# Optimization experiments

Measured on AMD Instinct MI355X. Metric: run time of the kernel, lower is better.

Reference implementation:

```python
import jax, jax.numpy as jnp
import numpy as np

B, T, D, H, d = 2, 2048, 1024, 16, 64
INNER = H * d
SCALE = d ** -0.5


def _rope(x, inv_freq):
    # x: [B, H, T, d], interleaved rotary as in the torch module
    t = x.shape[2]
    pos = jnp.arange(t, dtype=jnp.float32)
    freqs = pos[:, None] * inv_freq[None, :]          # [T, d/2]
    cos_f, sin_f = jnp.cos(freqs), jnp.sin(freqs)
    x1, x2 = x[..., 0::2], x[..., 1::2]
    y1 = x1 * cos_f - x2 * sin_f
    y2 = x1 * sin_f + x2 * cos_f
    return jnp.stack([y1, y2], axis=-1).reshape(x.shape)


def setup_inputs() -> dict:
    key = jax.random.key(0)
    ks = jax.random.split(key, 6)
    x = jax.random.normal(ks[0], (B, T, D), jnp.float32)
    W_qkv = jax.random.normal(ks[1], (D, 3 * INNER), jnp.float32) * (D ** -0.5)
    W_out = jax.random.normal(ks[2], (INNER, D), jnp.float32) * (INNER ** -0.5)
    W_dt = jax.random.normal(ks[3], (D, H), jnp.float32) * 0.01
    b_dt = jnp.full((H,), -4.0, jnp.float32)
    W_gsp = jax.random.normal(ks[4], (D, INNER), jnp.float32) * 0.01
    b_gsp = jnp.full((INNER,), -3.0, jnp.float32)
    inv_freq = 1.0 / (10000.0 ** (jnp.arange(0, d, 2, dtype=jnp.float32) / d))
    return {"x": x, "W_qkv": W_qkv, "W_out": W_out, "W_dt": W_dt,
            "b_dt": b_dt, "W_gsp": W_gsp, "b_gsp": b_gsp, "inv_freq": inv_freq}


def reference(x, W_qkv, W_out, W_dt, b_dt, W_gsp, b_gsp, inv_freq):
    qkv = (x @ W_qkv).reshape(B, T, 3, H, d)
    Q = jnp.moveaxis(qkv[:, :, 0], 1, 2)   # [B,H,T,d]
    K = jnp.moveaxis(qkv[:, :, 1], 1, 2)
    V = jnp.moveaxis(qkv[:, :, 2], 1, 2)
    Q = _rope(Q, inv_freq)
    K = _rope(K, inv_freq)

    dt = jax.nn.softplus(x @ W_dt + b_dt)             # [B,T,H]
    gamma = jnp.moveaxis(jnp.exp(-dt), 1, 2)          # [B,H,T]

    p = jax.nn.sigmoid(x @ W_gsp + b_gsp).reshape(B, T, H, d)
    p = jnp.moveaxis(p, 1, 2)                          # [B,H,T,d]
    gamma_eff = gamma[..., None] * (1.0 - p) + p
    gamma_scalar = gamma_eff.mean(axis=-1)            # [B,H,T]
    V = V * (1.0 - p)

    log_gamma = jnp.log(jnp.clip(gamma_scalar, 1e-6, 1.0 - 1e-6))
    lgc = jnp.cumsum(log_gamma, axis=-1)              # [B,H,T]
    log_D = jnp.clip(lgc[..., :, None] - lgc[..., None, :], -20.0, 0.0)
    causal = jnp.tril(jnp.ones((T, T), jnp.float32))
    Dm = jnp.exp(log_D) * causal                      # [B,H,T,T]

    Wscore = jnp.einsum('bhtd,bhsd->bhts', Q * SCALE, K)
    A = Wscore * Dm
    Y = jnp.einsum('bhts,bhsd->bhtd', A, V)
    Y = jnp.moveaxis(Y, 1, 2).reshape(B, T, INNER)
    return Y @ W_out
```

## Files before the change

### kernel.cpp

```cpp
#include <hip/hip_runtime.h>
#include <hip/hip_bf16.h>
#include <math.h>

#define B_     2
#define T_     2048
#define D_     1024
#define H_     16
#define INNER_ 1024
#define NC_    4096
#define SCALE_ 0.125f

typedef unsigned short u16;
typedef short short8 __attribute__((ext_vector_type(8)));
typedef float f32x4 __attribute__((ext_vector_type(4)));
typedef unsigned short u16x4 __attribute__((ext_vector_type(4)));

__device__ __forceinline__ u16 f2bf(float x) {
  union { float f; unsigned u; } v; v.f = x;
  unsigned r = v.u + 0x7fffu + ((v.u >> 16) & 1u);
  return (u16)(r >> 16);
}
__device__ __forceinline__ float b2f(u16 x) {
  union { unsigned u; float f; } v; v.u = ((unsigned)x) << 16;
  return v.f;
}
__device__ __forceinline__ void gload16(const void* g, void* l) {
  __builtin_amdgcn_global_load_lds(
      (const __attribute__((address_space(1))) void*)g,
      (__attribute__((address_space(3))) void*)l, 16, 0, 0);
}

__global__ __launch_bounds__(256) void prep_kernel(
    const float* __restrict__ x, const float* __restrict__ W_qkv,
    const float* __restrict__ W_gsp, const float* __restrict__ W_out,
    const float* __restrict__ W_dt, const float* __restrict__ inv_freq,
    u16* __restrict__ xb, u16* __restrict__ Wcombt, u16* __restrict__ Woutt,
    u16* __restrict__ Wdtb, float2* __restrict__ tab) {
  const int bid = blockIdx.x, tid = threadIdx.x;
  if (bid < 1280) {
    const float* src; u16* dst; int N, nx, ky;
    if (bid < 768)       { src = W_qkv; dst = Wcombt;                N = 3072; nx = bid % 48;          ky = bid / 48; }
    else if (bid < 1024) { src = W_gsp; dst = Wcombt + 3072 * 1024;  N = 1024; nx = (bid - 768) % 16;  ky = (bid - 768) / 16; }
    else                 { src = W_out; dst = Woutt;                 N = 1024; nx = (bid - 1024) % 16; ky = (bid - 1024) / 16; }
    __shared__ float tile[64][65];
    const int k0 = ky * 64, n0 = nx * 64;
    for (int e = tid; e < 4096; e += 256) {
      int kk = e >> 6, nn = e & 63;
      tile[kk][nn] = src[(size_t)(k0 + kk) * N + n0 + nn];
    }
    __syncthreads();
    for (int e = tid; e < 4096; e += 256) {
      int nn = e >> 6, kk = e & 63;
      dst[(size_t)(n0 + nn) * 1024 + k0 + kk] = f2bf(tile[kk][nn]);
    }
  } else if (bid < 1344) {
    int i = (bid - 1280) * 256 + tid;
    int k = i >> 4, h = i & 15;
    Wdtb[(size_t)h * D_ + k] = f2bf(W_dt[i]);
  } else if (bid < 1600) {
    int i = (bid - 1344) * 256 + tid;
    int t = i >> 5, j = i & 31;
    float s, c;
    sincosf((float)t * inv_freq[j], &s, &c);
    tab[i] = make_float2(c, s);
  } else {
    int base = (bid - 1600) * 1024 + tid;
#pragma unroll
    for (int r = 0; r < 4; ++r) {
      int i = base + r * 256;
      float4 v = *reinterpret_cast<const float4*>(x + (size_t)i * 4);
      u16x4 o; o.x = f2bf(v.x); o.y = f2bf(v.y); o.z = f2bf(v.z); o.w = f2bf(v.w);
      *reinterpret_cast<u16x4*>(xb + (size_t)i * 4) = o;
    }
  }
}

__global__ __launch_bounds__(256) void gamma_kernel(
    const u16* __restrict__ xb, const u16* __restrict__ Wdtb,
    const float* __restrict__ b_dt, float* __restrict__ gam) {
  const int row = blockIdx.x * 4 + (threadIdx.x >> 6);
  const int l = threadIdx.x & 63;
  const int h = l >> 2;
  const int kc = (l & 3) * 256;
  const short8* xp = (const short8*)(xb + (size_t)row * D_ + kc);
  const short8* wp = (const short8*)(Wdtb + h * D_ + kc);
  float s = 0.f;
#pragma unroll
  for (int i = 0; i < 32; ++i) {
    short8 xv = xp[i], wv = wp[i];
#pragma unroll
    for (int j = 0; j < 8; ++j) s += b2f((u16)xv[j]) * b2f((u16)wv[j]);
  }
  s += __shfl_xor(s, 1);
  s += __shfl_xor(s, 2);
  if ((l & 3) == 0) {
    float v = s + b_dt[h];
    float sp = (v > 20.f) ? v : log1pf(__expf(v));
    gam[row * H_ + h] = __expf(-sp);
  }
}

#define SWZG(r) ((((r) & 3) ^ (((r) >> 2) & 1)))

__device__ __forceinline__ void stage_op(const u16* __restrict__ gbase, int kt,
                                         char* ldst, int h, int tid) {
  int r = h * 128 + (tid >> 2);
  int kg = (tid & 3) ^ SWZG(r);
  gload16(gbase + (size_t)r * D_ + kt * 32 + kg * 8,
          ldst + (h * 128 + (tid >> 6) * 16) * 64);
}
__device__ __forceinline__ short8 ldfrag(const char* tile, int row, int g4) {
  return *(const short8*)(tile + row * 64 + ((g4 ^ SWZG(row)) << 4));
}

__global__ __launch_bounds__(512, 2) void gemm_big(
    const u16* __restrict__ A, const u16* __restrict__ Bt,
    u16* __restrict__ C) {
  __shared__ char lds[4 * 32768];
  const int tid = threadIdx.x;
  const int w = tid >> 6, l = tid & 63;
  const int bid = blockIdx.x;
  const int xcd = bid & 7, idx = bid >> 3;
  const int brow = (xcd >> 1) * 4 + (idx & 3);
  const int bcol = (xcd & 1) * 8 + (idx >> 2);
  const int m0 = brow * 256, n0 = bcol * 256;
  const int wr = (w >> 2) * 128, wc = (w & 3) * 64;
  const int ql = l & 15, g4 = l >> 4;

  const u16* Ag = A + (size_t)m0 * D_;
  const u16* Bg = Bt + (size_t)n0 * D_;

  f32x4 acc[8][4] = {};

#pragma unroll
  for (int t = 0; t < 3; ++t) {
    char* bufA = lds + t * 32768;
    char* bufB = bufA + 16384;
    stage_op(Ag, t, bufA, 0, tid); stage_op(Ag, t, bufA, 1, tid);
    stage_op(Bg, t, bufB, 0, tid); stage_op(Bg, t, bufB, 1, tid);
  }

  const int NT = D_ / 32;
  for (int kt = 0; kt < NT; ++kt) {
    if (kt < NT - 2)       asm volatile("s_waitcnt vmcnt(8)" ::: "memory");
    else if (kt == NT - 2) asm volatile("s_waitcnt vmcnt(4)" ::: "memory");
    else                   asm volatile("s_waitcnt vmcnt(0)" ::: "memory");
    __builtin_amdgcn_sched_barrier(0);
    __builtin_amdgcn_s_barrier();
    __builtin_amdgcn_sched_barrier(0);

    char* bufA = lds + (kt & 3) * 32768;
    char* bufB = bufA + 16384;
    char* nbufA = lds + ((kt + 3) & 3) * 32768;
    char* nbufB = nbufA + 16384;
    const bool pre = (kt + 3 < NT);

    if (pre) {
      stage_op(Ag, kt + 3, nbufA, 0, tid);
      stage_op(Ag, kt + 3, nbufA, 1, tid);
    }
    short8 bf[4];
#pragma unroll
    for (int nf = 0; nf < 4; ++nf) bf[nf] = ldfrag(bufB, wc + nf * 16 + ql, g4);
    short8 af[4];
#pragma unroll
    for (int mf = 0; mf < 4; ++mf) af[mf] = ldfrag(bufA, wr + mf * 16 + ql, g4);
    __builtin_amdgcn_s_setprio(1);
#pragma unroll
    for (int mf = 0; mf < 4; ++mf)
#pragma unroll
      for (int nf = 0; nf < 4; ++nf)
        acc[mf][nf] = __builtin_amdgcn_mfma_f32_16x16x32_bf16(af[mf], bf[nf], acc[mf][nf], 0, 0, 0);
    __builtin_amdgcn_s_setprio(0);

    if (pre) {
      stage_op(Bg, kt + 3, nbufB, 0, tid);
      stage_op(Bg, kt + 3, nbufB, 1, tid);
    }
    short8 af2[4];
#pragma unroll
    for (int mf = 0; mf < 4; ++mf) af2[mf] = ldfrag(bufA, wr + 64 + mf * 16 + ql, g4);
    __builtin_amdgcn_s_setprio(1);
#pragma unroll
    for (int mf = 0; mf < 4; ++mf)
#pragma unroll
      for (int nf = 0; nf < 4; ++nf)
        acc[mf + 4][nf] = __builtin_amdgcn_mfma_f32_16x16x32_bf16(af2[mf], bf[nf], acc[mf + 4][nf], 0, 0, 0);
    __builtin_amdgcn_s_setprio(0);
  }

#pragma unroll
  for (int mf = 0; mf < 8; ++mf) {
#pragma unroll
    for (int r = 0; r < 4; ++r) {
      size_t row = (size_t)(m0 + wr + mf * 16 + g4 * 4 + r);
      size_t base = row * NC_ + n0 + wc + ql;
#pragma unroll
      for (int nf = 0; nf < 4; ++nf)
        C[base + nf * 16] = f2bf(acc[mf][nf][r]);
    }
  }
}

template <bool BF16OUT>
__global__ __launch_bounds__(256) void gemm_bt(
    const u16* __restrict__ A, const u16* __restrict__ Bt,
    void* __restrict__ Cv, int M, int N, int K) {
  __shared__ u16 As[2][128 * 64] __attribute__((aligned(16)));
  __shared__ u16 Bs[2][128 * 64] __attribute__((aligned(16)));
  const int tid = threadIdx.x, w = tid >> 6, l = tid & 63;
  const int rpx = (M >> 7) >> 3;
  const int bid = blockIdx.x;
  const int xcd = bid & 7, idx = bid >> 3;
  const int brow = xcd * rpx + (idx % rpx);
  const int bcol = idx / rpx;
  const int m0 = brow * 128, n0 = bcol * 128;
  const int wr = (w >> 1) * 64, wc = (w & 1) * 64;
  const int srow = l >> 3;
  const int kgrp = ((l & 7) ^ srow) * 8;

  f32x4 acc[4][4] = {};

  auto stage = [&](int kt, int bs) {
#pragma unroll
    for (int i = 0; i < 4; ++i) {
      int c = w * 4 + i;
      int row = c * 8 + srow;
      gload16(A + (size_t)(m0 + row) * K + kt * 64 + kgrp, (char*)As[bs] + c * 1024);
      gload16(Bt + (size_t)(n0 + row) * K + kt * 64 + kgrp, (char*)Bs[bs] + c * 1024);
    }
  };

  stage(0, 0);
  const int NT = K >> 6;
  for (int kt = 0; kt < NT; ++kt) {
    if (kt + 1 < NT) {
      stage(kt + 1, (kt + 1) & 1);
      asm volatile("s_waitcnt vmcnt(8)" ::: "memory");
    } else {
      asm volatile("s_waitcnt vmcnt(0)" ::: "memory");
    }
    __builtin_amdgcn_sched_barrier(0);
    __builtin_amdgcn_s_barrier();
    __builtin_amdgcn_sched_barrier(0);
    const char* Asb = (const char*)As[kt & 1];
    const char* Bsb = (const char*)Bs[kt & 1];
#pragma unroll
    for (int kk = 0; kk < 2; ++kk) {
      short8 af[4], bf[4];
#pragma unroll
      for (int i = 0; i < 4; ++i) {
        int ra = wr + i * 16 + (l & 15);
        int sa = kk * 4 + (l >> 4);
        af[i] = *(const short8*)(Asb + ra * 128 + ((sa ^ (ra & 7)) << 4));
        int rb = wc + i * 16 + (l & 15);
        bf[i] = *(const short8*)(Bsb + rb * 128 + ((sa ^ (rb & 7)) << 4));
      }
#pragma unroll
      for (int i = 0; i < 4; ++i)
#pragma unroll
        for (int j = 0; j < 4; ++j)
          acc[i][j] = __builtin_amdgcn_mfma_f32_16x16x32_bf16(af[i], bf[j], acc[i][j], 0, 0, 0);
    }
    if (kt + 1 < NT) __builtin_amdgcn_s_barrier();
  }
#pragma unroll
  for (int i = 0; i < 4; ++i) {
#pragma unroll
    for (int r = 0; r < 4; ++r) {
      size_t row = (size_t)(m0 + wr + i * 16 + (l >> 4) * 4 + r);
      size_t base = row * N + n0 + wc + (l & 15);
#pragma unroll
      for (int j = 0; j < 4; ++j) {
        if (BF16OUT) ((u16*)Cv)[base + j * 16] = f2bf(acc[i][j][r]);
        else         ((float*)Cv)[base + j * 16] = acc[i][j][r];
      }
    }
  }
}

__global__ __launch_bounds__(256) void pointwise_kernel(
    const u16* __restrict__ C, const float* __restrict__ gam,
    const float* __restrict__ b_gsp, const float2* __restrict__ tab,
    u16* __restrict__ Qb, u16* __restrict__ Kb, u16* __restrict__ Vb,
    float* __restrict__ lg) {
  const int row = blockIdx.x * 4 + (threadIdx.x >> 6);
  const int l = threadIdx.x & 63;
  const int b = row >> 11, t = row & (T_ - 1);
  const int h = l >> 2;
  const int dd0 = (l & 3) * 16;
  const int col = h * 64 + dd0;
  const size_t cb = (size_t)row * NC_;

  const float gh = gam[row * H_ + h];
  const short8* qp = (const short8*)(C + cb + col);
  const short8* kp = (const short8*)(C + cb + 1024 + col);
  const short8* vp = (const short8*)(C + cb + 2048 + col);
  const short8* pp = (const short8*)(C + cb + 3072 + col);
  short8 q0 = qp[0], q1 = qp[1];
  short8 k0 = kp[0], k1 = kp[1];
  short8 v0 = vp[0], v1 = vp[1];
  short8 pr0 = pp[0], pr1 = pp[1];

  float ge = 0.f;
  short8 vo0, vo1;
#pragma unroll
  for (int i = 0; i < 8; ++i) {
    float pv = b2f((u16)pr0[i]) + b_gsp[col + i];
    float p = 1.f / (1.f + __expf(-pv));
    ge += gh * (1.f - p) + p;
    vo0[i] = (short)f2bf(b2f((u16)v0[i]) * (1.f - p));
    float pv1 = b2f((u16)pr1[i]) + b_gsp[col + 8 + i];
    float p1 = 1.f / (1.f + __expf(-pv1));
    ge += gh * (1.f - p1) + p1;
    vo1[i] = (short)f2bf(b2f((u16)v1[i]) * (1.f - p1));
  }
  const size_t hm = (((size_t)(b * H_ + h)) * T_ + t) * 64 + dd0;
  ((short8*)(Vb + hm))[0] = vo0;
  ((short8*)(Vb + hm))[1] = vo1;

  ge += __shfl_xor(ge, 1);
  ge += __shfl_xor(ge, 2);
  if ((l & 3) == 0) {
    float gs = ge * (1.f / 64.f);
    gs = fminf(fmaxf(gs, 1e-6f), 1.f - 1e-6f);
    lg[((size_t)(b * H_ + h)) * T_ + t] = logf(gs);
  }

  short8 qo0, qo1, ko0, ko1;
  const float2* cs = tab + t * 32 + (dd0 >> 1);
#pragma unroll
  for (int m = 0; m < 4; ++m) {
    float2 c0 = cs[m];
    float qa = b2f((u16)q0[2 * m]), qb = b2f((u16)q0[2 * m + 1]);
    qo0[2 * m]     = (short)f2bf((qa * c0.x - qb * c0.y) * SCALE_);
    qo0[2 * m + 1] = (short)f2bf((qa * c0.y + qb * c0.x) * SCALE_);
    float ka = b2f((u16)k0[2 * m]), kb = b2f((u16)k0[2 * m + 1]);
    ko0[2 * m]     = (short)f2bf(ka * c0.x - kb * c0.y);
    ko0[2 * m + 1] = (short)f2bf(ka * c0.y + kb * c0.x);
    float2 c1 = cs[4 + m];
    float qa1 = b2f((u16)q1[2 * m]), qb1 = b2f((u16)q1[2 * m + 1]);
    qo1[2 * m]     = (short)f2bf((qa1 * c1.x - qb1 * c1.y) * SCALE_);
    qo1[2 * m + 1] = (short)f2bf((qa1 * c1.y + qb1 * c1.x) * SCALE_);
    float ka1 = b2f((u16)k1[2 * m]), kb1 = b2f((u16)k1[2 * m + 1]);
    ko1[2 * m]     = (short)f2bf(ka1 * c1.x - kb1 * c1.y);
    ko1[2 * m + 1] = (short)f2bf(ka1 * c1.y + kb1 * c1.x);
  }
  ((short8*)(Qb + hm))[0] = qo0; ((short8*)(Qb + hm))[1] = qo1;
  ((short8*)(Kb + hm))[0] = ko0; ((short8*)(Kb + hm))[1] = ko1;
}

__global__ __launch_bounds__(256) void scan_kernel(
    const float* __restrict__ lg, float* __restrict__ lgc) {
  const size_t base = (size_t)blockIdx.x * T_;
  const int tid = threadIdx.x;
  __shared__ float sums[256];
  float loc[8];
  float run = 0.f;
#pragma unroll
  for (int i = 0; i < 8; ++i) { run += lg[base + tid * 8 + i]; loc[i] = run; }
  sums[tid] = run;
  __syncthreads();
  if (tid == 0) {
    float r = 0.f;
    for (int i = 0; i < 256; ++i) { float v = sums[i]; sums[i] = r; r += v; }
  }
  __syncthreads();
  const float off = sums[tid];
#pragma unroll
  for (int i = 0; i < 8; ++i) lgc[base + tid * 8 + i] = off + loc[i];
}

__global__ __launch_bounds__(256) void kv_prep_kernel(
    const u16* __restrict__ Vb, const float* __restrict__ lgc,
    u16* __restrict__ Vtg) {
  const int stile = blockIdx.x;
  const int bh = blockIdx.y;
  const int tid = threadIdx.x;
  __shared__ u16 vt[64][72];
  const size_t base = ((size_t)bh * T_ + (size_t)stile * 64) * 64;
  const float* lgp = lgc + (size_t)bh * T_;
  const float lgb = lgp[stile * 64];
#pragma unroll
  for (int i = 0; i < 2; ++i) {
    int c = tid * 2 + i;
    int row = c >> 3, k8 = (c & 7) * 8;
    float beta = __expf(lgb - lgp[stile * 64 + row]);
    short8 vv = *(const short8*)(Vb + base + row * 64 + k8);
#pragma unroll
    for (int j = 0; j < 8; ++j) vt[row][k8 + j] = f2bf(b2f((u16)vv[j]) * beta);
  }
  __syncthreads();
#pragma unroll
  for (int i = 0; i < 2; ++i) {
    int c = tid * 2 + i;
    int dd = c >> 3, t8 = (c & 7) * 8;
    short8 o;
#pragma unroll
    for (int j = 0; j < 8; ++j) o[j] = (short)vt[t8 + j][dd];
    *(short8*)(Vtg + ((size_t)bh * 64 + dd) * T_ + stile * 64 + t8) = o;
  }
}

__global__ __launch_bounds__(256) void attn_mfma(
    const u16* __restrict__ Qb, const u16* __restrict__ Kb,
    const u16* __restrict__ Vtg, const float* __restrict__ lgc,
    u16* __restrict__ Y) {
  const int i = blockIdx.x;
  const int tt = (i >> 3) & 31;
  const int bh = (i & 7) + ((i >> 8) << 3);
  const int b = bh >> 4, h = bh & 15;
  const int tid = threadIdx.x, w = tid >> 6, l = tid & 63;
  __shared__ u16 Qs[64 * 64] __attribute__((aligned(16)));
  __shared__ u16 Ks[2][64 * 64] __attribute__((aligned(16)));
  __shared__ u16 Vs[2][64 * 64] __attribute__((aligned(16)));
  const u16* Qg = Qb + (size_t)bh * T_ * 64;
  const u16* Kg = Kb + (size_t)bh * T_ * 64;
  const u16* Vg = Vtg + (size_t)bh * 64 * T_;
  const float* lgp = lgc + (size_t)bh * T_;

  const int srow = l >> 3;
  const int kgrp = ((l & 7) ^ srow) * 8;
  const int ql = l & 15, g4 = l >> 4;

#pragma unroll
  for (int i2 = 0; i2 < 2; ++i2) {
    int c = w * 2 + i2;
    int row = c * 8 + srow;
    gload16(Qg + (size_t)(tt * 64 + row) * 64 + kgrp, (char*)Qs + c * 1024);
  }
  const float lgq = lgp[tt * 64 + w * 16 + ql];
  const float lgtop = lgp[tt * 64];
  __syncthreads();

  short8 qf[2];
#pragma unroll
  for (int kk = 0; kk < 2; ++kk) {
    int row = w * 16 + ql;
    int slot = kk * 4 + g4;
    qf[kk] = *(const short8*)((const char*)Qs + row * 128 + ((slot ^ (row & 7)) << 4));
  }
  char* Pw = (char*)Qs + w * 2048;
  const int pswz = (ql & 7) << 4;

  f32x4 yacc[4] = {};

  {
    const int bs = tt & 1;
#pragma unroll
    for (int i2 = 0; i2 < 2; ++i2) {
      int c = w * 2 + i2, row = c * 8 + srow;
      gload16(Kg + (size_t)(tt * 64 + row) * 64 + kgrp, (char*)Ks[bs] + c * 1024);
      gload16(Vg + (size_t)row * T_ + tt * 64 + kgrp, (char*)Vs[bs] + c * 1024);
    }
  }

  for (int st = tt;; --st) {
    const int bs = st & 1;
    const bool last = (st == 0) || (lgtop - lgp[(st - 1) * 64 + 63] <= -20.f);
    if (!last) {
#pragma unroll
      for (int i2 = 0; i2 < 2; ++i2) {
        int c = w * 2 + i2, row = c * 8 + srow;
        gload16(Kg + (size_t)((st - 1) * 64 + row) * 64 + kgrp, (char*)Ks[bs ^ 1] + c * 1024);
        gload16(Vg + (size_t)row * T_ + (st - 1) * 64 + kgrp, (char*)Vs[bs ^ 1] + c * 1024);
      }
      asm volatile("s_waitcnt vmcnt(4)" ::: "memory");
    } else {
      asm volatile("s_waitcnt vmcnt(0)" ::: "memory");
    }
    __builtin_amdgcn_sched_barrier(0);
    __builtin_amdgcn_s_barrier();
    __builtin_amdgcn_sched_barrier(0);

    const float alpha = __expf(lgq - lgp[st * 64]);
    const bool diag = (st == tt);
    const char* Ksb = (const char*)Ks[bs];
    const char* Vsb = (const char*)Vs[bs];
#pragma unroll
    for (int n = 0; n < 4; ++n) {
      f32x4 s = {};
#pragma unroll
      for (int kk = 0; kk < 2; ++kk) {
        int row = n * 16 + ql;
        int slot = kk * 4 + g4;
        short8 kf = *(const short8*)(Ksb + row * 128 + ((slot ^ (row & 7)) << 4));
        s = __builtin_amdgcn_mfma_f32_16x16x32_bf16(kf, qf[kk], s, 0, 0, 0);
      }
      u16x4 pk;
#pragma unroll
      for (int r = 0; r < 4; ++r) {
        float pv = s[r] * alpha;
        if (diag && (n * 16 + g4 * 4 + r) > (w * 16 + ql)) pv = 0.f;
        pk[r] = f2bf(pv);
      }
      *(u16x4*)(Pw + ((ql * 128 + n * 32 + g4 * 8) ^ pswz)) = pk;
    }
#pragma unroll
    for (int kk = 0; kk < 2; ++kk) {
      short8 pf = *(const short8*)(Pw + ((ql * 128 + kk * 64 + g4 * 16) ^ pswz));
#pragma unroll
      for (int n2 = 0; n2 < 4; ++n2) {
        int row = n2 * 16 + ql;
        int slot = kk * 4 + g4;
        short8 vf = *(const short8*)(Vsb + row * 128 + ((slot ^ (row & 7)) << 4));
        yacc[n2] = __builtin_amdgcn_mfma_f32_16x16x32_bf16(pf, vf, yacc[n2], 0, 0, 0);
      }
    }
    if (last) break;
    __builtin_amdgcn_s_barrier();
  }

#pragma unroll
  for (int n2 = 0; n2 < 4; ++n2)
#pragma unroll
    for (int r = 0; r < 4; ++r) {
      size_t row = (size_t)(b * T_) + tt * 64 + w * 16 + g4 * 4 + r;
      Y[row * INNER_ + h * 64 + n2 * 16 + ql] = f2bf(yacc[n2][r]);
    }
}

extern "C" void kernel_launch(void* const* d_in, const int* in_sizes, int n_in,
                              void* d_out, int out_size, void* d_ws, size_t ws_size,
                              hipStream_t stream) {
  const float* x        = (const float*)d_in[0];
  const float* W_qkv    = (const float*)d_in[1];
  const float* W_out    = (const float*)d_in[2];
  const float* W_dt     = (const float*)d_in[3];
  const float* b_dt     = (const float*)d_in[4];
  const float* W_gsp    = (const float*)d_in[5];
  const float* b_gsp    = (const float*)d_in[6];
  const float* inv_freq = (const float*)d_in[7];
  float* out = (float*)d_out;

  const int M = B_ * T_;
  char* p = (char*)d_ws;
  auto alloc = [&](size_t bytes) {
    char* r = p; p += (bytes + 255) & ~(size_t)255; return r;
  };
  u16*    xb    = (u16*)alloc((size_t)M * D_ * 2);
  u16*    Wcombt= (u16*)alloc((size_t)NC_ * D_ * 2);
  u16*    Woutt = (u16*)alloc((size_t)D_ * INNER_ * 2);
  u16*    Wdtb  = (u16*)alloc((size_t)H_ * D_ * 2);
  u16*    Cqkvp = (u16*)alloc((size_t)M * NC_ * 2);
  u16*    Qb    = (u16*)alloc((size_t)B_ * H_ * T_ * 64 * 2);
  u16*    Kb    = (u16*)alloc((size_t)B_ * H_ * T_ * 64 * 2);
  u16*    Vb    = (u16*)alloc((size_t)B_ * H_ * T_ * 64 * 2);
  float*  gam   = (float*)alloc((size_t)M * H_ * 4);
  float*  lg    = (float*)alloc((size_t)B_ * H_ * T_ * 4);
  float*  lgc   = (float*)alloc((size_t)B_ * H_ * T_ * 4);
  float2* tab   = (float2*)alloc((size_t)T_ * 32 * 8);
  u16*    Vtg   = Cqkvp;
  u16*    Yb    = Cqkvp + (size_t)4 * 1024 * 1024;

  prep_kernel<<<2624, 256, 0, stream>>>(x, W_qkv, W_gsp, W_out, W_dt, inv_freq,
                                        xb, Wcombt, Woutt, Wdtb, tab);
  gamma_kernel<<<M / 4, 256, 0, stream>>>(xb, Wdtb, b_dt, gam);
  gemm_big<<<256, 512, 0, stream>>>(xb, Wcombt, Cqkvp);

  pointwise_kernel<<<M / 4, 256, 0, stream>>>(Cqkvp, gam, b_gsp, tab,
                                              Qb, Kb, Vb, lg);
  scan_kernel<<<B_ * H_, 256, 0, stream>>>(lg, lgc);
  kv_prep_kernel<<<dim3(T_ / 64, B_ * H_), 256, 0, stream>>>(Vb, lgc, Vtg);

  attn_mfma<<<1024, 256, 0, stream>>>(Qb, Kb, Vtg, lgc, Yb);

  gemm_bt<false><<<256, 256, 0, stream>>>(Yb, Woutt, out, M, D_, INNER_);
}
```

Baseline: 156.2 us.

## Load K/V fragments directly from global into registers, drop LDS staging

The attention kernel no longer stages Q, K and V tiles through shared memory with double buffering and block barriers. Each wave now loads its MFMA operand fragments straight from global memory into registers, and the V-transpose kernel writes V in a tiled [bh][tile][d][64] layout so those loads are contiguous. It also raises wave priority around MFMA sections. This removes the LDS traffic and barriers, but gives up explicit prefetch overlap and has every wave re-read the full K/V tiles from global memory or cache.

```diff
diff --git a/kernel.cpp b/kernel.cpp
--- a/kernel.cpp
+++ b/kernel.cpp
@@ -398,7 +398,7 @@
     short8 o;
 #pragma unroll
     for (int j = 0; j < 8; ++j) o[j] = (short)vt[t8 + j][dd];
-    *(short8*)(Vtg + ((size_t)bh * 64 + dd) * T_ + stile * 64 + t8) = o;
+    *(short8*)(Vtg + ((size_t)(bh * 32 + stile) * 64 + dd) * 64 + t8) = o;
   }
 }
 
@@ -411,82 +411,47 @@
   const int bh = (i & 7) + ((i >> 8) << 3);
   const int b = bh >> 4, h = bh & 15;
   const int tid = threadIdx.x, w = tid >> 6, l = tid & 63;
-  __shared__ u16 Qs[64 * 64] __attribute__((aligned(16)));
-  __shared__ u16 Ks[2][64 * 64] __attribute__((aligned(16)));
-  __shared__ u16 Vs[2][64 * 64] __attribute__((aligned(16)));
+  __shared__ u16 Ps[4][1024];
   const u16* Qg = Qb + (size_t)bh * T_ * 64;
   const u16* Kg = Kb + (size_t)bh * T_ * 64;
-  const u16* Vg = Vtg + (size_t)bh * 64 * T_;
+  const u16* Vg = Vtg + (size_t)bh * 32 * 4096;
   const float* lgp = lgc + (size_t)bh * T_;
-
-  const int srow = l >> 3;
-  const int kgrp = ((l & 7) ^ srow) * 8;
   const int ql = l & 15, g4 = l >> 4;
 
-#pragma unroll
-  for (int i2 = 0; i2 < 2; ++i2) {
-    int c = w * 2 + i2;
-    int row = c * 8 + srow;
-    gload16(Qg + (size_t)(tt * 64 + row) * 64 + kgrp, (char*)Qs + c * 1024);
-  }
+  const u16* qptr = Qg + (size_t)(tt * 64 + w * 16 + ql) * 64 + g4 * 8;
+  const short8 qf0 = *(const short8*)(qptr);
+  const short8 qf1 = *(const short8*)(qptr + 32);
   const float lgq = lgp[tt * 64 + w * 16 + ql];
   const float lgtop = lgp[tt * 64];
-  __syncthreads();
-
-  short8 qf[2];
-#pragma unroll
-  for (int kk = 0; kk < 2; ++kk) {
-    int row = w * 16 + ql;
-    int slot = kk * 4 + g4;
-    qf[kk] = *(const short8*)((const char*)Qs + row * 128 + ((slot ^ (row & 7)) << 4));
-  }
-  char* Pw = (char*)Qs + w * 2048;
+
+  char* Pw = (char*)Ps[w];
   const int pswz = (ql & 7) << 4;
 
   f32x4 yacc[4] = {};
 
-  {
-    const int bs = tt & 1;
-#pragma unroll
-    for (int i2 = 0; i2 < 2; ++i2) {
-      int c = w * 2 + i2, row = c * 8 + srow;
-      gload16(Kg + (size_t)(tt * 64 + row) * 64 + kgrp, (char*)Ks[bs] + c * 1024);
-      gload16(Vg + (size_t)row * T_ + tt * 64 + kgrp, (char*)Vs[bs] + c * 1024);
-    }
-  }
-
-  for (int st = tt;; --st) {
-    const int bs = st & 1;
-    const bool last = (st == 0) || (lgtop - lgp[(st - 1) * 64 + 63] <= -20.f);
-    if (!last) {
-#pragma unroll
-      for (int i2 = 0; i2 < 2; ++i2) {
-        int c = w * 2 + i2, row = c * 8 + srow;
-        gload16(Kg + (size_t)((st - 1) * 64 + row) * 64 + kgrp, (char*)Ks[bs ^ 1] + c * 1024);
-        gload16(Vg + (size_t)row * T_ + (st - 1) * 64 + kgrp, (char*)Vs[bs ^ 1] + c * 1024);
-      }
-      asm volatile("s_waitcnt vmcnt(4)" ::: "memory");
-    } else {
-      asm volatile("s_waitcnt vmcnt(0)" ::: "memory");
-    }
-    __builtin_amdgcn_sched_barrier(0);
-    __builtin_amdgcn_s_barrier();
-    __builtin_amdgcn_sched_barrier(0);
-
+  for (int st = tt; st >= 0; --st) {
+    if (st < tt && lgtop - lgp[st * 64 + 63] <= -20.f) break;
+    const u16* kb = Kg + (size_t)st * 64 * 64;
+    const u16* vb = Vg + (size_t)st * 4096;
+    short8 kf[4][2], vf[4][2];
+#pragma unroll
+    for (int n = 0; n < 4; ++n) {
+      const u16* kr = kb + (n * 16 + ql) * 64 + g4 * 8;
+      kf[n][0] = *(const short8*)(kr);
+      kf[n][1] = *(const short8*)(kr + 32);
+      const u16* vr = vb + (n * 16 + ql) * 64 + g4 * 8;
+      vf[n][0] = *(const short8*)(vr);
+      vf[n][1] = *(const short8*)(vr + 32);
+    }
     const float alpha = __expf(lgq - lgp[st * 64]);
     const bool diag = (st == tt);
-    const char* Ksb = (const char*)Ks[bs];
-    const char* Vsb = (const char*)Vs[bs];
 #pragma unroll
     for (int n = 0; n < 4; ++n) {
       f32x4 s = {};
-#pragma unroll
-      for (int kk = 0; kk < 2; ++kk) {
-        int row = n * 16 + ql;
-        int slot = kk * 4 + g4;
-        short8 kf = *(const short8*)(Ksb + row * 128 + ((slot ^ (row & 7)) << 4));
-        s = __builtin_amdgcn_mfma_f32_16x16x32_bf16(kf, qf[kk], s, 0, 0, 0);
-      }
+      __builtin_amdgcn_s_setprio(1);
+      s = __builtin_amdgcn_mfma_f32_16x16x32_bf16(kf[n][0], qf0, s, 0, 0, 0);
+      s = __builtin_amdgcn_mfma_f32_16x16x32_bf16(kf[n][1], qf1, s, 0, 0, 0);
+      __builtin_amdgcn_s_setprio(0);
       u16x4 pk;
 #pragma unroll
       for (int r = 0; r < 4; ++r) {
@@ -499,16 +464,12 @@
 #pragma unroll
     for (int kk = 0; kk < 2; ++kk) {
       short8 pf = *(const short8*)(Pw + ((ql * 128 + kk * 64 + g4 * 16) ^ pswz));
-#pragma unroll
-      for (int n2 = 0; n2 < 4; ++n2) {
-        int row = n2 * 16 + ql;
-        int slot = kk * 4 + g4;
-        short8 vf = *(const short8*)(Vsb + row * 128 + ((slot ^ (row & 7)) << 4));
-        yacc[n2] = __builtin_amdgcn_mfma_f32_16x16x32_bf16(pf, vf, yacc[n2], 0, 0, 0);
-      }
-    }
-    if (last) break;
-    __builtin_amdgcn_s_barrier();
+      __builtin_amdgcn_s_setprio(1);
+#pragma unroll
+      for (int n2 = 0; n2 < 4; ++n2)
+        yacc[n2] = __builtin_amdgcn_mfma_f32_16x16x32_bf16(pf, vf[n2][kk], yacc[n2], 0, 0, 0);
+      __builtin_amdgcn_s_setprio(0);
+    }
   }
 
 #pragma unroll
```

After: 255.3 us. +63.5%, slower.

## Use 32x32 MFMA with 128-row query tiles and tiled V layout in attention

Applied to the files above, without the earlier changes.

The attention kernel now handles 128 query rows per block (32 per wave) using 32x32x16 bf16 MFMA instead of 16x16x32, which halves the grid and lets each loaded K/V tile serve twice as many queries. Q fragments are loaded straight from global memory instead of being staged through LDS. The transposed V buffer is rewritten as contiguous 64x64 tiles so each tile is read from one contiguous 8 KB region. Fully masked diagonal tiles are skipped and s_setprio hints wrap the MFMA sections. The trade-off is more registers per wave and fewer blocks in flight for the causal workload.

```diff
diff --git a/kernel.cpp b/kernel.cpp
--- a/kernel.cpp
+++ b/kernel.cpp
@@ -13,6 +13,7 @@
 typedef unsigned short u16;
 typedef short short8 __attribute__((ext_vector_type(8)));
 typedef float f32x4 __attribute__((ext_vector_type(4)));
+typedef float f32x16 __attribute__((ext_vector_type(16)));
 typedef unsigned short u16x4 __attribute__((ext_vector_type(4)));
 
 __device__ __forceinline__ u16 f2bf(float x) {
@@ -398,7 +399,7 @@
     short8 o;
 #pragma unroll
     for (int j = 0; j < 8; ++j) o[j] = (short)vt[t8 + j][dd];
-    *(short8*)(Vtg + ((size_t)bh * 64 + dd) * T_ + stile * 64 + t8) = o;
+    *(short8*)(Vtg + ((size_t)(bh * 32 + stile) * 64 + dd) * 64 + t8) = o;
   }
 }
 
@@ -407,63 +408,57 @@
     const u16* __restrict__ Vtg, const float* __restrict__ lgc,
     u16* __restrict__ Y) {
   const int i = blockIdx.x;
-  const int tt = (i >> 3) & 31;
-  const int bh = (i & 7) + ((i >> 8) << 3);
+  const int xcd = i & 7, r = i >> 3;
+  const int qb = r & 15;
+  const int bh = xcd + ((r >> 4) << 3);
   const int b = bh >> 4, h = bh & 15;
   const int tid = threadIdx.x, w = tid >> 6, l = tid & 63;
-  __shared__ u16 Qs[64 * 64] __attribute__((aligned(16)));
+  const int l31 = l & 31, hi = l >> 5;
   __shared__ u16 Ks[2][64 * 64] __attribute__((aligned(16)));
   __shared__ u16 Vs[2][64 * 64] __attribute__((aligned(16)));
+  __shared__ u16 Ps[4][2048] __attribute__((aligned(16)));
   const u16* Qg = Qb + (size_t)bh * T_ * 64;
   const u16* Kg = Kb + (size_t)bh * T_ * 64;
-  const u16* Vg = Vtg + (size_t)bh * 64 * T_;
+  const u16* Vg = Vtg + (size_t)bh * 32 * 4096;
   const float* lgp = lgc + (size_t)bh * T_;
-
-  const int srow = l >> 3;
-  const int kgrp = ((l & 7) ^ srow) * 8;
-  const int ql = l & 15, g4 = l >> 4;
-
-#pragma unroll
-  for (int i2 = 0; i2 < 2; ++i2) {
-    int c = w * 2 + i2;
-    int row = c * 8 + srow;
-    gload16(Qg + (size_t)(tt * 64 + row) * 64 + kgrp, (char*)Qs + c * 1024);
-  }
-  const float lgq = lgp[tt * 64 + w * 16 + ql];
-  const float lgtop = lgp[tt * 64];
-  __syncthreads();
-
-  short8 qf[2];
-#pragma unroll
-  for (int kk = 0; kk < 2; ++kk) {
-    int row = w * 16 + ql;
-    int slot = kk * 4 + g4;
-    qf[kk] = *(const short8*)((const char*)Qs + row * 128 + ((slot ^ (row & 7)) << 4));
-  }
-  char* Pw = (char*)Qs + w * 2048;
-  const int pswz = (ql & 7) << 4;
-
-  f32x4 yacc[4] = {};
-
+  const int srow = l >> 3, slot8 = l & 7;
+
+  const int q0 = qb * 128 + w * 32;
+  const int qg = q0 + l31;
+  short8 qf[4];
+#pragma unroll
+  for (int kk = 0; kk < 4; ++kk)
+    qf[kk] = *(const short8*)(Qg + (size_t)qg * 64 + kk * 16 + hi * 8);
+  const float lgq = lgp[qg];
+  const float lgtop = lgp[qb * 128];
+
+  char* Pw = (char*)Ps[w];
+  const int psw = l31 & 7;
+
+  f32x16 yacc0 = {}, yacc1 = {};
+
+  const int st0 = qb * 2 + 1;
   {
-    const int bs = tt & 1;
+    const int bs = st0 & 1;
 #pragma unroll
     for (int i2 = 0; i2 < 2; ++i2) {
       int c = w * 2 + i2, row = c * 8 + srow;
-      gload16(Kg + (size_t)(tt * 64 + row) * 64 + kgrp, (char*)Ks[bs] + c * 1024);
-      gload16(Vg + (size_t)row * T_ + tt * 64 + kgrp, (char*)Vs[bs] + c * 1024);
-    }
-  }
-
-  for (int st = tt;; --st) {
+      int kg = (slot8 ^ (row & 7)) * 8;
+      gload16(Kg + (size_t)(st0 * 64 + row) * 64 + kg, (char*)Ks[bs] + c * 1024);
+      gload16(Vg + (size_t)st0 * 4096 + row * 64 + kg, (char*)Vs[bs] + c * 1024);
+    }
+  }
+
+  for (int st = st0;; --st) {
     const int bs = st & 1;
     const bool last = (st == 0) || (lgtop - lgp[(st - 1) * 64 + 63] <= -20.f);
     if (!last) {
 #pragma unroll
       for (int i2 = 0; i2 < 2; ++i2) {
         int c = w * 2 + i2, row = c * 8 + srow;
-        gload16(Kg + (size_t)((st - 1) * 64 + row) * 64 + kgrp, (char*)Ks[bs ^ 1] + c * 1024);
-        gload16(Vg + (size_t)row * T_ + (st - 1) * 64 + kgrp, (char*)Vs[bs ^ 1] + c * 1024);
+        int kg = (slot8 ^ (row & 7)) * 8;
+        gload16(Kg + (size_t)((st - 1) * 64 + row) * 64 + kg, (char*)Ks[bs ^ 1] + c * 1024);
+        gload16(Vg + (size_t)(st - 1) * 4096 + row * 64 + kg, (char*)Vs[bs ^ 1] + c * 1024);
       }
       asm volatile("s_waitcnt vmcnt(4)" ::: "memory");
     } else {
@@ -473,38 +468,47 @@
     __builtin_amdgcn_s_barrier();
     __builtin_amdgcn_sched_barrier(0);
 
-    const float alpha = __expf(lgq - lgp[st * 64]);
-    const bool diag = (st == tt);
-    const char* Ksb = (const char*)Ks[bs];
-    const char* Vsb = (const char*)Vs[bs];
-#pragma unroll
-    for (int n = 0; n < 4; ++n) {
-      f32x4 s = {};
-#pragma unroll
-      for (int kk = 0; kk < 2; ++kk) {
-        int row = n * 16 + ql;
-        int slot = kk * 4 + g4;
-        short8 kf = *(const short8*)(Ksb + row * 128 + ((slot ^ (row & 7)) << 4));
-        s = __builtin_amdgcn_mfma_f32_16x16x32_bf16(kf, qf[kk], s, 0, 0, 0);
+    const bool allinv = (st * 64 > q0 + 31);
+    if (!allinv) {
+      const char* Ksb = (const char*)Ks[bs];
+      const char* Vsb = (const char*)Vs[bs];
+      const float alpha = __expf(lgq - lgp[st * 64]);
+      const bool domask = (st * 64 + 63 > q0);
+      const int qrel = qg - st * 64;
+#pragma unroll
+      for (int sblk = 0; sblk < 2; ++sblk) {
+        f32x16 c = {};
+        __builtin_amdgcn_s_setprio(1);
+#pragma unroll
+        for (int kk = 0; kk < 4; ++kk) {
+          int row = sblk * 32 + l31;
+          short8 kf = *(const short8*)(Ksb + row * 128 + (((kk * 2 + hi) ^ (row & 7)) << 4));
+          c = __builtin_amdgcn_mfma_f32_32x32x16_bf16(kf, qf[kk], c, 0, 0, 0);
+        }
+        __builtin_amdgcn_s_setprio(0);
+#pragma unroll
+        for (int bq = 0; bq < 4; ++bq) {
+          u16x4 pk;
+#pragma unroll
+          for (int r2 = 0; r2 < 4; ++r2) {
+            int s64 = sblk * 32 + bq * 8 + hi * 4 + r2;
+            float pv = c[bq * 4 + r2] * alpha;
+            if (domask && s64 > qrel) pv = 0.f;
+            pk[r2] = f2bf(pv);
+          }
+          int slot = sblk * 4 + bq;
+          *(u16x4*)(Pw + l31 * 128 + ((slot ^ psw) << 4) + hi * 8) = pk;
+        }
       }
-      u16x4 pk;
-#pragma unroll
-      for (int r = 0; r < 4; ++r) {
-        float pv = s[r] * alpha;
-        if (diag && (n * 16 + g4 * 4 + r) > (w * 16 + ql)) pv = 0.f;
-        pk[r] = f2bf(pv);
-      }
-      *(u16x4*)(Pw + ((ql * 128 + n * 32 + g4 * 8) ^ pswz)) = pk;
-    }
-#pragma unroll
-    for (int kk = 0; kk < 2; ++kk) {
-      short8 pf = *(const short8*)(Pw + ((ql * 128 + kk * 64 + g4 * 16) ^ pswz));
-#pragma unroll
-      for (int n2 = 0; n2 < 4; ++n2) {
-        int row = n2 * 16 + ql;
-        int slot = kk * 4 + g4;
-        short8 vf = *(const short8*)(Vsb + row * 128 + ((slot ^ (row & 7)) << 4));
-        yacc[n2] = __builtin_amdgcn_mfma_f32_16x16x32_bf16(pf, vf, yacc[n2], 0, 0, 0);
+#pragma unroll
+      for (int kk = 0; kk < 4; ++kk) {
+        short8 pf = *(const short8*)(Pw + l31 * 128 + (((kk * 2 + hi) ^ psw) << 4));
+        short8 vf0 = *(const short8*)(Vsb + l31 * 128 + (((kk * 2 + hi) ^ (l31 & 7)) << 4));
+        short8 vf1 = *(const short8*)(Vsb + (32 + l31) * 128 + (((kk * 2 + hi) ^ (l31 & 7)) << 4));
+        __builtin_amdgcn_s_setprio(1);
+        yacc0 = __builtin_amdgcn_mfma_f32_32x32x16_bf16(pf, vf0, yacc0, 0, 0, 0);
+        yacc1 = __builtin_amdgcn_mfma_f32_32x32x16_bf16(pf, vf1, yacc1, 0, 0, 0);
+        __builtin_amdgcn_s_setprio(0);
       }
     }
     if (last) break;
@@ -512,12 +516,12 @@
   }
 
 #pragma unroll
-  for (int n2 = 0; n2 < 4; ++n2)
-#pragma unroll
-    for (int r = 0; r < 4; ++r) {
-      size_t row = (size_t)(b * T_) + tt * 64 + w * 16 + g4 * 4 + r;
-      Y[row * INNER_ + h * 64 + n2 * 16 + ql] = f2bf(yacc[n2][r]);
-    }
+  for (int reg = 0; reg < 16; ++reg) {
+    int qrow = (reg & 3) + 8 * (reg >> 2) + 4 * hi;
+    size_t rowg = (size_t)(b * T_) + qb * 128 + w * 32 + qrow;
+    Y[rowg * INNER_ + h * 64 + l31] = f2bf(yacc0[reg]);
+    Y[rowg * INNER_ + h * 64 + 32 + l31] = f2bf(yacc1[reg]);
+  }
 }
 
 extern "C" void kernel_launch(void* const* d_in, const int* in_sizes, int n_in,
@@ -563,7 +567,7 @@
   scan_kernel<<<B_ * H_, 256, 0, stream>>>(lg, lgc);
   kv_prep_kernel<<<dim3(T_ / 64, B_ * H_), 256, 0, stream>>>(Vb, lgc, Vtg);
 
-  attn_mfma<<<1024, 256, 0, stream>>>(Qb, Kb, Vtg, lgc, Yb);
+  attn_mfma<<<512, 256, 0, stream>>>(Qb, Kb, Vtg, lgc, Yb);
 
   gemm_bt<false><<<256, 256, 0, stream>>>(Yb, Woutt, out, M, D_, INNER_);
 }
```

New measurement: 159.7 us. 1.02x slower.
